# Performance work log

Hardware: AMD Instinct MI355X
Metric: run time of the kernel (lower is better)

Reference implementation:

```python
import jax, jax.numpy as jnp
import numpy as np

D_MODEL = 768
D_STATE = 16
D_CONV = 4
EXPAND = 2
D_INNER = D_MODEL * EXPAND  # 1536
B = 2
T = 8192
ALPHA = 0.9  # hard-coded EMA coefficient in _parallel_scan


def setup_inputs() -> dict:
    key = jax.random.key(0)
    ks = jax.random.split(key, 12)
    s = 0.02
    return {
        "x": jax.random.normal(ks[0], (B, T, D_MODEL), jnp.float32),
        "in_w": jax.random.normal(ks[1], (D_MODEL, 2 * D_INNER), jnp.float32) * s,
        "in_b": jnp.zeros((2 * D_INNER,), jnp.float32),
        "conv_w": jax.random.normal(ks[2], (D_INNER, 1, D_CONV), jnp.float32) * s,  # OIH, depthwise
        "conv_b": jnp.zeros((D_INNER,), jnp.float32),
        "xp_w": jax.random.normal(ks[3], (D_INNER, 2 * D_STATE), jnp.float32) * s,
        "xp_b": jnp.zeros((2 * D_STATE,), jnp.float32),
        "dt_w": jax.random.normal(ks[4], (D_STATE, D_INNER), jnp.float32) * s,
        "dt_b": jnp.zeros((D_INNER,), jnp.float32),
        "D_param": jnp.ones((D_INNER,), jnp.float32),
        "out_w": jax.random.normal(ks[5], (D_INNER, D_MODEL), jnp.float32) * s,
        "out_b": jnp.zeros((D_MODEL,), jnp.float32),
    }


def _forward(x, in_w, in_b, conv_w, conv_b, xp_w, xp_b, dt_w, dt_b, D_param, out_w, out_b):
    # in_proj: [B,T,D] -> [B,T,2*d_inner]
    xz = x @ in_w + in_b
    x_inner, z = jnp.split(xz, 2, axis=-1)

    # Causal depthwise conv1d (torch pads both sides by d_conv-1 then slices [:T],
    # which is equivalent to left-pad d_conv-1, right-pad 0)
    xc = jnp.transpose(x_inner, (0, 2, 1))  # [B, d_inner, T]
    xc = jax.lax.conv_general_dilated(
        xc, conv_w, window_strides=(1,), padding=[(D_CONV - 1, 0)],
        dimension_numbers=("NCH", "OIH", "NCH"), feature_group_count=D_INNER,
    ) + conv_b[None, :, None]
    x_conv = jax.nn.silu(jnp.transpose(xc, (0, 2, 1)))  # [B, T, d_inner]

    # NOTE: original computes x_proj/dt_proj/A_bar here, but _parallel_scan ignores
    # A_bar/B_ssm/C_ssm entirely, so they are dead code w.r.t. the output (omitted).

    # Serial EMA scan: h_t = alpha*h_{t-1} + (1-alpha)*x_conv_t
    def step(h, xt):
        h = ALPHA * h + (1.0 - ALPHA) * xt
        return h, h

    h0 = jnp.zeros((x.shape[0], D_INNER), x_conv.dtype)
    _, hs = jax.lax.scan(step, h0, jnp.transpose(x_conv, (1, 0, 2)))  # [T,B,d_inner]
    scan_out = jnp.transpose(hs, (1, 0, 2))

    y = x_conv * D_param + scan_out
    y = y * jax.nn.silu(z)
    return y @ out_w + out_b  # dropout is identity at inference


def reference(x, in_w, in_b, conv_w, conv_b, xp_w, xp_b, dt_w, dt_b, D_param, out_w, out_b):
    return _forward(x, in_w, in_b, conv_w, conv_b, xp_w, xp_b, dt_w, dt_b, D_param, out_w, out_b)
```

## Files before the change

### kernel.cpp

```cpp
#include <hip/hip_runtime.h>

#define D_MODEL 768
#define D_INNER 1536
#define NXZ     3072
#define BATCH   2
#define SEQ     8192
#define MTOT    (BATCH*SEQ)
#define WARM    64

typedef _Float16 v8h __attribute__((ext_vector_type(8)));
typedef _Float16 v4h __attribute__((ext_vector_type(4)));
typedef float    v4f __attribute__((ext_vector_type(4)));
typedef _Float16 f16;

__global__ void k_cvt(const float* __restrict__ in, f16* __restrict__ out, int n4) {
  int i = blockIdx.x * blockDim.x + threadIdx.x;
  if (i < n4) {
    float4 v = reinterpret_cast<const float4*>(in)[i];
    v4h o;
    o[0] = (f16)v.x; o[1] = (f16)v.y; o[2] = (f16)v.z; o[3] = (f16)v.w;
    reinterpret_cast<v4h*>(out)[i] = o;
  }
}

__global__ void k_transpose_cvt(const float* __restrict__ in, f16* __restrict__ out,
                                int R, int C) {
  __shared__ float tile[32][33];
  int c0 = blockIdx.x * 32, r0 = blockIdx.y * 32;
  int tx = threadIdx.x, ty = threadIdx.y;
#pragma unroll
  for (int i = 0; i < 32; i += 8)
    tile[ty + i][tx] = in[(long)(r0 + ty + i) * C + (c0 + tx)];
  __syncthreads();
#pragma unroll
  for (int i = 0; i < 32; i += 8)
    out[(long)(c0 + ty + i) * R + (r0 + tx)] = (f16)tile[tx][ty + i];
}

__device__ __forceinline__ void gload_lds16(const void* g, void* l) {
  __builtin_amdgcn_global_load_lds((const __attribute__((address_space(1))) void*)g,
                                   (__attribute__((address_space(3))) void*)l, 16, 0, 0);
}

template <bool F16OUT>
__launch_bounds__(256, 2)
__global__ void k_gemm_bt(const f16* __restrict__ A, const f16* __restrict__ Bt,
                          const float* __restrict__ bias, void* __restrict__ Cv,
                          int M, int N, int K) {
  __shared__ f16 As[128][64];
  __shared__ f16 Bs[128][64];
  const int tid  = threadIdx.x;
  const int lane = tid & 63;
  const int wave = tid >> 6;
  const int wm   = (wave >> 1) * 64;
  const int wn   = (wave & 1) * 64;
  const int m16  = lane & 15;
  const int quad = lane >> 4;
  const long m0 = (long)blockIdx.y * 128;
  const long n0 = (long)blockIdx.x * 128;

  v4f acc[4][4];
#pragma unroll
  for (int i = 0; i < 4; i++)
#pragma unroll
    for (int j = 0; j < 4; j++)
#pragma unroll
      for (int r = 0; r < 4; r++) acc[i][j][r] = 0.f;

  const int  srow = wave * 8 + (lane >> 3);
  const int  gcol = ((lane & 7) ^ (lane >> 3)) << 3;
  const f16* Ag = A  + (m0 + srow) * (long)K + gcol;
  const f16* Bg = Bt + (n0 + srow) * (long)K + gcol;
  f16* AsD0 = &As[wave * 8][0];
  f16* AsD1 = &As[wave * 8 + 32][0];
  f16* AsD2 = &As[wave * 8 + 64][0];
  f16* AsD3 = &As[wave * 8 + 96][0];
  f16* BsD0 = &Bs[wave * 8][0];
  f16* BsD1 = &Bs[wave * 8 + 32][0];
  f16* BsD2 = &Bs[wave * 8 + 64][0];
  f16* BsD3 = &Bs[wave * 8 + 96][0];

  const int c0q = ((quad ^ (m16 & 7)) << 3);
  const int c1q = c0q ^ 32;

  for (int k0 = 0; k0 < K; k0 += 64) {
    gload_lds16(Ag,                AsD0);
    gload_lds16(Ag + (long)32 * K, AsD1);
    gload_lds16(Ag + (long)64 * K, AsD2);
    gload_lds16(Ag + (long)96 * K, AsD3);
    gload_lds16(Bg,                BsD0);
    gload_lds16(Bg + (long)32 * K, BsD1);
    gload_lds16(Bg + (long)64 * K, BsD2);
    gload_lds16(Bg + (long)96 * K, BsD3);
    Ag += 64; Bg += 64;
    __syncthreads();
    v8h af[4], bfr[4];
#pragma unroll
    for (int i = 0; i < 4; i++) af[i]  = *(const v8h*)&As[wm + i * 16 + m16][c0q];
#pragma unroll
    for (int j = 0; j < 4; j++) bfr[j] = *(const v8h*)&Bs[wn + j * 16 + m16][c0q];
#pragma unroll
    for (int i = 0; i < 4; i++)
#pragma unroll
      for (int j = 0; j < 4; j++)
        acc[i][j] = __builtin_amdgcn_mfma_f32_16x16x32_f16(af[i], bfr[j], acc[i][j], 0, 0, 0);
#pragma unroll
    for (int i = 0; i < 4; i++) af[i]  = *(const v8h*)&As[wm + i * 16 + m16][c1q];
#pragma unroll
    for (int j = 0; j < 4; j++) bfr[j] = *(const v8h*)&Bs[wn + j * 16 + m16][c1q];
#pragma unroll
    for (int i = 0; i < 4; i++)
#pragma unroll
      for (int j = 0; j < 4; j++)
        acc[i][j] = __builtin_amdgcn_mfma_f32_16x16x32_f16(af[i], bfr[j], acc[i][j], 0, 0, 0);
    __syncthreads();
  }

#pragma unroll
  for (int i = 0; i < 4; i++) {
#pragma unroll
    for (int j = 0; j < 4; j++) {
      const long n = n0 + wn + j * 16 + m16;
      const float bv = bias[n];
#pragma unroll
      for (int r = 0; r < 4; r++) {
        const long m = m0 + wm + i * 16 + quad * 4 + r;
        float v = acc[i][j][r] + bv;
        if (F16OUT) ((f16*)Cv)[m * N + n] = (f16)v;
        else        ((float*)Cv)[m * N + n] = v;
      }
    }
  }
}

__global__ void k_conv_scan(const f16* __restrict__ xz, const float* __restrict__ conv_w,
                            const float* __restrict__ conv_b, const float* __restrict__ Dp_,
                            f16* __restrict__ y) {
  __shared__ f16 xs[64][256];
  __shared__ f16 zs[64][256];
  const int tid = threadIdx.x;
  const int c0  = blockIdx.y * 256;
  const int c   = c0 + tid;
  const int b   = blockIdx.z;
  const int t0  = blockIdx.x * 128;
  const float w0 = conv_w[c * 4 + 0], w1 = conv_w[c * 4 + 1];
  const float w2 = conv_w[c * 4 + 2], w3 = conv_w[c * 4 + 3];
  const float cb = conv_b[c], Dp = Dp_[c];
  const long mb = (long)b * SEQ;

  float xm3 = 0.f, xm2 = 0.f, xm1 = 0.f, h = 0.f;
  const int ts = t0 - WARM;
  if (t0 > 0) {
    xm3 = (float)xz[(mb + ts - 3) * (long)NXZ + c];
    xm2 = (float)xz[(mb + ts - 2) * (long)NXZ + c];
    xm1 = (float)xz[(mb + ts - 1) * (long)NXZ + c];
  }

  for (int p = 0; p < 3; ++p) {
    const int tp = ts + p * 64;
    __syncthreads();
    if (tp >= 0) {
#pragma unroll
      for (int j = 0; j < 8; ++j) {
        const int idx = j * 256 + tid, row = idx >> 5, col = (idx & 31) << 3;
        *(v8h*)&xs[row][col] = *(const v8h*)&xz[(mb + tp + row) * (long)NXZ + c0 + col];
      }
      if (p > 0) {
#pragma unroll
        for (int j = 0; j < 8; ++j) {
          const int idx = j * 256 + tid, row = idx >> 5, col = (idx & 31) << 3;
          *(v8h*)&zs[row][col] = *(const v8h*)&xz[(mb + tp + row) * (long)NXZ + D_INNER + c0 + col];
        }
      }
    }
    __syncthreads();
    if (tp < 0) continue;
    if (p == 0) {
      for (int tl = 0; tl < 64; ++tl) {
        float xt = (float)xs[tl][tid];
        float u = w0 * xm3 + w1 * xm2 + w2 * xm1 + w3 * xt + cb;
        h = 0.9f * h + 0.1f * (u / (1.f + __expf(-u)));
        xm3 = xm2; xm2 = xm1; xm1 = xt;
      }
    } else {
      f16* yo = y + (mb + tp) * (long)D_INNER + c;
      for (int tl = 0; tl < 64; ++tl) {
        float xt = (float)xs[tl][tid];
        float u = w0 * xm3 + w1 * xm2 + w2 * xm1 + w3 * xt + cb;
        float v = u / (1.f + __expf(-u));
        h = 0.9f * h + 0.1f * v;
        float zv = (float)zs[tl][tid];
        float g = zv / (1.f + __expf(-zv));
        yo[(long)tl * D_INNER] = (f16)((v * Dp + h) * g);
        xm3 = xm2; xm2 = xm1; xm1 = xt;
      }
    }
  }
}

extern "C" void kernel_launch(void* const* d_in, const int* in_sizes, int n_in,
                              void* d_out, int out_size, void* d_ws, size_t ws_size,
                              hipStream_t stream) {
  const float* x       = (const float*)d_in[0];
  const float* in_w    = (const float*)d_in[1];
  const float* in_b    = (const float*)d_in[2];
  const float* conv_w  = (const float*)d_in[3];
  const float* conv_b  = (const float*)d_in[4];
  const float* D_param = (const float*)d_in[9];
  const float* out_w   = (const float*)d_in[10];
  const float* out_b   = (const float*)d_in[11];
  float* out = (float*)d_out;

  char* p = (char*)d_ws;
  f16* xb    = (f16*)p; p += (size_t)MTOT * D_MODEL * 2;
  f16* wInT  = (f16*)p; p += (size_t)NXZ * D_MODEL * 2;
  f16* wOutT = (f16*)p; p += (size_t)D_MODEL * D_INNER * 2;
  f16* xzb   = (f16*)p; p += (size_t)MTOT * NXZ * 2;
  f16* yb    = (f16*)p; p += (size_t)MTOT * D_INNER * 2;

  k_cvt<<<(MTOT * D_MODEL / 4 + 255) / 256, 256, 0, stream>>>(x, xb, MTOT * D_MODEL / 4);
  k_transpose_cvt<<<dim3(NXZ / 32, D_MODEL / 32), dim3(32, 8), 0, stream>>>(in_w, wInT, D_MODEL, NXZ);
  k_transpose_cvt<<<dim3(D_MODEL / 32, D_INNER / 32), dim3(32, 8), 0, stream>>>(out_w, wOutT, D_INNER, D_MODEL);

  k_gemm_bt<true><<<dim3(NXZ / 128, MTOT / 128), 256, 0, stream>>>(xb, wInT, in_b, xzb, MTOT, NXZ, D_MODEL);

  k_conv_scan<<<dim3(SEQ / 128, D_INNER / 256, BATCH), 256, 0, stream>>>(xzb, conv_w, conv_b, D_param, yb);

  k_gemm_bt<false><<<dim3(D_MODEL / 128, MTOT / 128), 256, 0, stream>>>(yb, wOutT, out_b, out, MTOT, D_MODEL, D_INNER);
}
```

Before: 339.3 us.

## Double-buffer LDS in input-projection GEMM to overlap global loads with MFMA

Adds a double-buffered GEMM variant that issues the direct-to-LDS global loads for the next K tile before computing on the current tile. It uses explicit vmcnt waits and barriers in place of the two full syncthreads per iteration. This is meant to hide global memory latency in the in_proj GEMM. LDS use doubles to 64KB per block, which may reduce occupancy. The output GEMM keeps the single-buffered kernel.

```diff
diff --git a/kernel.cpp b/kernel.cpp
--- a/kernel.cpp
+++ b/kernel.cpp
@@ -71,27 +71,16 @@
   const int  gcol = ((lane & 7) ^ (lane >> 3)) << 3;
   const f16* Ag = A  + (m0 + srow) * (long)K + gcol;
   const f16* Bg = Bt + (n0 + srow) * (long)K + gcol;
-  f16* AsD0 = &As[wave * 8][0];
-  f16* AsD1 = &As[wave * 8 + 32][0];
-  f16* AsD2 = &As[wave * 8 + 64][0];
-  f16* AsD3 = &As[wave * 8 + 96][0];
-  f16* BsD0 = &Bs[wave * 8][0];
-  f16* BsD1 = &Bs[wave * 8 + 32][0];
-  f16* BsD2 = &Bs[wave * 8 + 64][0];
-  f16* BsD3 = &Bs[wave * 8 + 96][0];
 
   const int c0q = ((quad ^ (m16 & 7)) << 3);
   const int c1q = c0q ^ 32;
 
   for (int k0 = 0; k0 < K; k0 += 64) {
-    gload_lds16(Ag,                AsD0);
-    gload_lds16(Ag + (long)32 * K, AsD1);
-    gload_lds16(Ag + (long)64 * K, AsD2);
-    gload_lds16(Ag + (long)96 * K, AsD3);
-    gload_lds16(Bg,                BsD0);
-    gload_lds16(Bg + (long)32 * K, BsD1);
-    gload_lds16(Bg + (long)64 * K, BsD2);
-    gload_lds16(Bg + (long)96 * K, BsD3);
+#pragma unroll
+    for (int g = 0; g < 4; ++g) {
+      gload_lds16(Ag + (long)(g * 32) * K, &As[wave * 8 + g * 32][0]);
+      gload_lds16(Bg + (long)(g * 32) * K, &Bs[wave * 8 + g * 32][0]);
+    }
     Ag += 64; Bg += 64;
     __syncthreads();
     v8h af[4], bfr[4];
@@ -115,6 +104,111 @@
         acc[i][j] = __builtin_amdgcn_mfma_f32_16x16x32_f16(af[i], bfr[j], acc[i][j], 0, 0, 0);
     __syncthreads();
   }
+
+#pragma unroll
+  for (int i = 0; i < 4; i++) {
+#pragma unroll
+    for (int j = 0; j < 4; j++) {
+      const long n = n0 + wn + j * 16 + m16;
+      const float bv = bias[n];
+#pragma unroll
+      for (int r = 0; r < 4; r++) {
+        const long m = m0 + wm + i * 16 + quad * 4 + r;
+        float v = acc[i][j][r] + bv;
+        if (F16OUT) ((f16*)Cv)[m * N + n] = (f16)v;
+        else        ((float*)Cv)[m * N + n] = v;
+      }
+    }
+  }
+}
+
+template <bool F16OUT>
+__launch_bounds__(256, 2)
+__global__ void k_gemm_db(const f16* __restrict__ A, const f16* __restrict__ Bt,
+                          const float* __restrict__ bias, void* __restrict__ Cv,
+                          int M, int N, int K) {
+  __shared__ f16 As[2][128][64];
+  __shared__ f16 Bs[2][128][64];
+  const int tid  = threadIdx.x;
+  const int lane = tid & 63;
+  const int wave = tid >> 6;
+  const int wm   = (wave >> 1) * 64;
+  const int wn   = (wave & 1) * 64;
+  const int m16  = lane & 15;
+  const int quad = lane >> 4;
+  const long m0 = (long)blockIdx.y * 128;
+  const long n0 = (long)blockIdx.x * 128;
+
+  v4f acc[4][4];
+#pragma unroll
+  for (int i = 0; i < 4; i++)
+#pragma unroll
+    for (int j = 0; j < 4; j++)
+#pragma unroll
+      for (int r = 0; r < 4; r++) acc[i][j][r] = 0.f;
+
+  const int  srow = wave * 8 + (lane >> 3);
+  const int  gcol = ((lane & 7) ^ (lane >> 3)) << 3;
+  const f16* Ag = A  + (m0 + srow) * (long)K + gcol;
+  const f16* Bg = Bt + (n0 + srow) * (long)K + gcol;
+
+  const int c0q = ((quad ^ (m16 & 7)) << 3);
+  const int c1q = c0q ^ 32;
+
+#define STAGE(BUF, KO)                                                        \
+  {                                                                           \
+    _Pragma("unroll")                                                         \
+    for (int g = 0; g < 4; ++g) {                                             \
+      gload_lds16(Ag + (KO) + (long)(g * 32) * K, &As[BUF][wave * 8 + g * 32][0]); \
+      gload_lds16(Bg + (KO) + (long)(g * 32) * K, &Bs[BUF][wave * 8 + g * 32][0]); \
+    }                                                                         \
+  }
+#define COMPUTE(BUF)                                                          \
+  {                                                                           \
+    v8h af[4], bfr[4];                                                        \
+    _Pragma("unroll")                                                         \
+    for (int i = 0; i < 4; i++) af[i]  = *(const v8h*)&As[BUF][wm + i * 16 + m16][c0q]; \
+    _Pragma("unroll")                                                         \
+    for (int j = 0; j < 4; j++) bfr[j] = *(const v8h*)&Bs[BUF][wn + j * 16 + m16][c0q]; \
+    _Pragma("unroll")                                                         \
+    for (int i = 0; i < 4; i++)                                               \
+      _Pragma("unroll")                                                       \
+      for (int j = 0; j < 4; j++)                                             \
+        acc[i][j] = __builtin_amdgcn_mfma_f32_16x16x32_f16(af[i], bfr[j], acc[i][j], 0, 0, 0); \
+    _Pragma("unroll")                                                         \
+    for (int i = 0; i < 4; i++) af[i]  = *(const v8h*)&As[BUF][wm + i * 16 + m16][c1q]; \
+    _Pragma("unroll")                                                         \
+    for (int j = 0; j < 4; j++) bfr[j] = *(const v8h*)&Bs[BUF][wn + j * 16 + m16][c1q]; \
+    _Pragma("unroll")                                                         \
+    for (int i = 0; i < 4; i++)                                               \
+      _Pragma("unroll")                                                       \
+      for (int j = 0; j < 4; j++)                                             \
+        acc[i][j] = __builtin_amdgcn_mfma_f32_16x16x32_f16(af[i], bfr[j], acc[i][j], 0, 0, 0); \
+  }
+
+  const int T = K >> 6;
+  STAGE(0, 0)
+
+  int t = 0;
+#pragma unroll 1
+  for (; t < T - 1; ++t) {
+    STAGE((t + 1) & 1, (t + 1) * 64)
+    asm volatile("s_waitcnt vmcnt(8)" ::: "memory");
+    __builtin_amdgcn_s_barrier();
+    __builtin_amdgcn_sched_barrier(0);
+    COMPUTE(t & 1)
+    asm volatile("s_waitcnt lgkmcnt(0)" ::: "memory");
+    __builtin_amdgcn_sched_barrier(0);
+    __builtin_amdgcn_s_barrier();
+    __builtin_amdgcn_sched_barrier(0);
+  }
+  asm volatile("s_waitcnt vmcnt(0)" ::: "memory");
+  __builtin_amdgcn_s_barrier();
+  __builtin_amdgcn_sched_barrier(0);
+  COMPUTE(t & 1)
+
+#undef STAGE
+#undef COMPUTE
 
 #pragma unroll
   for (int i = 0; i < 4; i++) {
@@ -222,7 +316,7 @@
   k_transpose_cvt<<<dim3(NXZ / 32, D_MODEL / 32), dim3(32, 8), 0, stream>>>(in_w, wInT, D_MODEL, NXZ);
   k_transpose_cvt<<<dim3(D_MODEL / 32, D_INNER / 32), dim3(32, 8), 0, stream>>>(out_w, wOutT, D_INNER, D_MODEL);
 
-  k_gemm_bt<true><<<dim3(NXZ / 128, MTOT / 128), 256, 0, stream>>>(xb, wInT, in_b, xzb, MTOT, NXZ, D_MODEL);
+  k_gemm_db<true><<<dim3(NXZ / 128, MTOT / 128), 256, 0, stream>>>(xb, wInT, in_b, xzb, MTOT, NXZ, D_MODEL);
 
   k_conv_scan<<<dim3(SEQ / 128, D_INNER / 256, BATCH), 256, 0, stream>>>(xzb, conv_w, conv_b, D_param, yb);
 
```

New measurement: 342.7 us. About the same (+1.0%).
